# Kernel tuning notes

Measured on AMD Instinct MI355X. Metric: run time of the kernel, lower is better.

Reference implementation:

```python
import jax, jax.numpy as jnp
import numpy as np

NUM_HEADS = 16
BLOCK = 64  # block_size = min(64, N)

def setup_inputs() -> dict:
    key = jax.random.key(0)
    k0, k1, k2 = jax.random.split(key, 3)
    B, N, C = 2, 2048, 1024
    x = jax.random.normal(k0, (B, N, C), dtype=jnp.float32)
    w_qkv = jax.random.normal(k1, (3 * C, C), dtype=jnp.float32) * 0.02  # torch Linear weight [out,in]
    w_proj = jax.random.normal(k2, (C, C), dtype=jnp.float32) * 0.02
    b_proj = jnp.zeros((C,), dtype=jnp.float32)
    return {"x": x, "w_qkv": w_qkv, "w_proj": w_proj, "b_proj": b_proj}

def reference(x, w_qkv, w_proj, b_proj):
    B, N, C = x.shape
    H = NUM_HEADS
    hd = C // H
    bs = min(BLOCK, N)
    scale = hd ** -0.5
    # qkv projection: [B,N,3C] -> [3,B,H,N,hd]
    qkv = (x @ w_qkv.T).reshape(B, N, 3, H, hd).transpose(2, 0, 3, 1, 4)
    q, k, v = qkv[0], qkv[1], qkv[2]
    # block-causal mask: query block i attends to all key blocks <= i
    blk = jnp.arange(N) // bs
    mask = blk[:, None] >= blk[None, :]  # [N,N]
    scores = jnp.einsum('bhqd,bhkd->bhqk', q, k) * scale
    scores = jnp.where(mask, scores, -jnp.inf)
    weights = jax.nn.softmax(scores, axis=-1)
    out = jnp.einsum('bhqk,bhkd->bhqd', weights, v)
    out = out.transpose(0, 2, 1, 3).reshape(B, N, C)
    return out @ w_proj.T + b_proj
```

## Files before the change

kernel.cpp:

```cpp
#include <hip/hip_runtime.h>

typedef __attribute__((ext_vector_type(8))) short bf16x8;
typedef __attribute__((ext_vector_type(4))) float f32x4;
typedef __attribute__((ext_vector_type(2))) unsigned int u32x2;
typedef __attribute__((ext_vector_type(8))) unsigned short ushort8v;

__device__ __forceinline__ unsigned short f2bf(float f) {
  unsigned int u = __float_as_uint(f);
  u += 0x7fffu + ((u >> 16) & 1u);
  return (unsigned short)(u >> 16);
}

__device__ __forceinline__ void gload_lds16(const unsigned short* g, unsigned short* l) {
  __builtin_amdgcn_global_load_lds(
      (const __attribute__((address_space(1))) unsigned int*)g,
      (__attribute__((address_space(3))) unsigned int*)l,
      16, 0, 0);
}

__global__ void cvt_all(const float* __restrict__ x, const float* __restrict__ wq,
                        const float* __restrict__ wp, unsigned short* __restrict__ dst) {
  const int n1 = 4096 * 1024 / 8, n2 = 3072 * 1024 / 8, n3 = 1024 * 1024 / 8;
  int stride = gridDim.x * blockDim.x;
  for (int i = blockIdx.x * blockDim.x + threadIdx.x; i < n1 + n2 + n3; i += stride) {
    const float* s; int j;
    if (i < n1)           { s = x;  j = i; }
    else if (i < n1 + n2) { s = wq; j = i - n1; }
    else                  { s = wp; j = i - n1 - n2; }
    float4 a = ((const float4*)s)[j * 2];
    float4 b = ((const float4*)s)[j * 2 + 1];
    ushort8v o;
    o[0] = f2bf(a.x); o[1] = f2bf(a.y); o[2] = f2bf(a.z); o[3] = f2bf(a.w);
    o[4] = f2bf(b.x); o[5] = f2bf(b.y); o[6] = f2bf(b.z); o[7] = f2bf(b.w);
    ((ushort8v*)dst)[i] = o;
  }
}

__device__ __forceinline__ void gemm128_bt(const unsigned short* __restrict__ A,
                                           const unsigned short* __restrict__ Bt,
                                           unsigned short* As, unsigned short* Bs,
                                           int tm, int tn, f32x4 acc[4][4]) {
  const int K = 1024;
  int tid = threadIdx.x;
  int w = tid >> 6, l = tid & 63;
  int wr = w >> 1, wc = w & 1;
  int g = l >> 4, c = l & 15;

  int srow = w * 32 + (l >> 2);
  int skoff = (((l & 3) ^ ((srow >> 1) & 3)) * 8);
  const unsigned short* gA = A + (size_t)(tm * 128 + srow) * K + skoff;
  const unsigned short* gB = Bt + (size_t)(tn * 128 + srow) * K + skoff;
  unsigned short* lA = As + (w * 32) * 32;
  unsigned short* lB = Bs + (w * 32) * 32;

  int rx = (c >> 1) & 3;
  int arow = wr * 64 + c;
  int brow = wc * 64 + c;

  for (int k0 = 0; k0 < K; k0 += 32) {
    gload_lds16(gA, lA);
    gload_lds16(gA + 16 * K, lA + 16 * 32);
    gload_lds16(gB, lB);
    gload_lds16(gB + 16 * K, lB + 16 * 32);
    gA += 32; gB += 32;
    __syncthreads();
    bf16x8 af[4], bfr[4];
#pragma unroll
    for (int mi = 0; mi < 4; ++mi)
      af[mi] = *(const bf16x8*)((const char*)As + (arow + mi * 16) * 64 + ((g ^ rx) << 4));
#pragma unroll
    for (int ni = 0; ni < 4; ++ni)
      bfr[ni] = *(const bf16x8*)((const char*)Bs + (brow + ni * 16) * 64 + ((g ^ rx) << 4));
#pragma unroll
    for (int mi = 0; mi < 4; ++mi)
#pragma unroll
      for (int ni = 0; ni < 4; ++ni)
        acc[mi][ni] = __builtin_amdgcn_mfma_f32_16x16x32_bf16(af[mi], bfr[ni], acc[mi][ni], 0, 0, 0);
    __syncthreads();
  }
}

__global__ __launch_bounds__(256) void qkv_gemm(const unsigned short* __restrict__ xb,
                                                const unsigned short* __restrict__ wb,
                                                unsigned short* __restrict__ Qp,
                                                unsigned short* __restrict__ Kp,
                                                unsigned short* __restrict__ Vt) {
  __shared__ unsigned short As[128 * 32];
  __shared__ unsigned short Bs[128 * 32];
  f32x4 acc[4][4];
#pragma unroll
  for (int i = 0; i < 4; ++i)
#pragma unroll
    for (int j = 0; j < 4; ++j) acc[i][j] = f32x4{0.f, 0.f, 0.f, 0.f};
  int id = (blockIdx.x & 7) * 96 + (blockIdx.x >> 3);
  int tm = id / 24, tn = id % 24;
  gemm128_bt(xb, wb, As, Bs, tm, tn, acc);

  int tid = threadIdx.x;
  int w = tid >> 6, l = tid & 63;
  int wr = w >> 1, wc = w & 1;
  int g = l >> 4, c = l & 15;
  const float QSCALE = 0.125f * 1.44269504088896f;
#pragma unroll
  for (int mi = 0; mi < 4; ++mi)
#pragma unroll
    for (int ni = 0; ni < 4; ++ni)
#pragma unroll
      for (int r = 0; r < 4; ++r) {
        int row = tm * 128 + wr * 64 + mi * 16 + g * 4 + r;
        int col = tn * 128 + wc * 64 + ni * 16 + c;
        int b = row >> 11, seq = row & 2047;
        int t = col >> 10;
        int h = (col >> 6) & 15, d = col & 63;
        size_t bh = (size_t)b * 16 + h;
        float v = acc[mi][ni][r];
        if (t == 0)      Qp[(bh * 2048 + seq) * 64 + d] = f2bf(v * QSCALE);
        else if (t == 1) Kp[(bh * 2048 + seq) * 64 + d] = f2bf(v);
        else             Vt[(bh * 64 + d) * 2048 + seq] = f2bf(v);
      }
}

__global__ __launch_bounds__(256, 3) void attn_fa(const unsigned short* __restrict__ Qp,
                                                  const unsigned short* __restrict__ Kp,
                                                  const unsigned short* __restrict__ Vt,
                                                  unsigned short* __restrict__ attn) {
  __shared__ unsigned short Ks[2][4096];
  __shared__ unsigned short Vs[2][4096];
  int tid = threadIdx.x;
  int w = tid >> 6, l = tid & 63;
  int g = l >> 4, c = l & 15;

  int idx = blockIdx.x;
  int pos = idx >> 3;
  int qb = 31 - (pos >> 2);
  int bh = (idx & 7) + 8 * (pos & 3);

  const unsigned short* Qbh = Qp + (size_t)bh * 2048 * 64;
  const unsigned short* Kbh = Kp + (size_t)bh * 2048 * 64;
  const unsigned short* Vbh = Vt + (size_t)bh * 64 * 2048;

  int rowA, colA, rowB, colB;
  { int L = tid * 16;         int P = L ^ (((L >> 7) & 7) << 4); rowA = P >> 7; colA = (P & 127) >> 1; }
  { int L = (tid + 256) * 16; int P = L ^ (((L >> 7) & 7) << 4); rowB = P >> 7; colB = (P & 127) >> 1; }
  const unsigned short* gKA = Kbh + rowA * 64 + colA;
  const unsigned short* gKB = Kbh + rowB * 64 + colB;
  const unsigned short* gVA = Vbh + (size_t)rowA * 2048 + colA;
  const unsigned short* gVB = Vbh + (size_t)rowB * 2048 + colB;

#define STAGE(buf, kb)                                              \
  do {                                                              \
    gload_lds16(gKA + (kb) * 4096, &Ks[(buf)][w * 512]);            \
    gload_lds16(gKB + (kb) * 4096, &Ks[(buf)][w * 512 + 2048]);     \
    gload_lds16(gVA + (kb) * 64,  &Vs[(buf)][w * 512]);             \
    gload_lds16(gVB + (kb) * 64,  &Vs[(buf)][w * 512 + 2048]);      \
  } while (0)

  bf16x8 qf[2];
  {
    size_t qrow = (size_t)qb * 64 + w * 16 + c;
    qf[0] = *(const bf16x8*)(Qbh + qrow * 64 + 8 * g);
    qf[1] = *(const bf16x8*)(Qbh + qrow * 64 + 32 + 8 * g);
  }

  float lp4[4] = {0.f, 0.f, 0.f, 0.f};
  f32x4 o[4];
#pragma unroll
  for (int df = 0; df < 4; ++df) o[df] = f32x4{0.f, 0.f, 0.f, 0.f};

  int xorv = c & 7;

  int cur = 0;
  STAGE(0, 0);
  __syncthreads();
  for (int kb = 0; kb <= qb; ++kb) {
    if (kb < qb) STAGE(1 - cur, kb + 1);

    const char* Kb = (const char*)&Ks[cur][0];
    const char* Vb = (const char*)&Vs[cur][0];
    bf16x8 kf[8];
#pragma unroll
    for (int nf = 0; nf < 4; ++nf) {
      int r = nf * 16 + c;
#pragma unroll
      for (int ks = 0; ks < 2; ++ks)
        kf[nf * 2 + ks] = *(const bf16x8*)(Kb + r * 128 + (((ks * 4 + g) ^ xorv) * 16));
    }
    f32x4 s4[4];
#pragma unroll
    for (int nf = 0; nf < 4; ++nf) {
      s4[nf] = f32x4{0.f, 0.f, 0.f, 0.f};
      s4[nf] = __builtin_amdgcn_mfma_f32_16x16x32_bf16(kf[nf * 2 + 0], qf[0], s4[nf], 0, 0, 0);
      s4[nf] = __builtin_amdgcn_mfma_f32_16x16x32_bf16(kf[nf * 2 + 1], qf[1], s4[nf], 0, 0, 0);
    }
    u32x2 pa[4];
#pragma unroll
    for (int nf = 0; nf < 4; ++nf) {
      float p0 = __builtin_amdgcn_exp2f(s4[nf][0]);
      float p1 = __builtin_amdgcn_exp2f(s4[nf][1]);
      float p2 = __builtin_amdgcn_exp2f(s4[nf][2]);
      float p3 = __builtin_amdgcn_exp2f(s4[nf][3]);
      lp4[nf] += (p0 + p1) + (p2 + p3);
      unsigned int w0, w1;
      asm("v_cvt_pk_bf16_f32 %0, %1, %2" : "=v"(w0) : "v"(p0), "v"(p1));
      asm("v_cvt_pk_bf16_f32 %0, %1, %2" : "=v"(w1) : "v"(p2), "v"(p3));
      pa[nf][0] = w0; pa[nf][1] = w1;
    }
#pragma unroll
    for (int df = 0; df < 4; ++df) {
      int vrow = df * 16 + c;
#pragma unroll
      for (int ks = 0; ks < 4; ++ks) {
        u32x2 vbf = *(const u32x2*)(Vb + vrow * 128 + (((2 * ks + (g >> 1)) ^ xorv) * 16) + 8 * (g & 1));
        asm("v_mfma_f32_16x16x16_bf16 %0, %1, %2, %0"
            : "+v"(o[df]) : "v"(pa[ks]), "v"(vbf));
      }
    }
    __syncthreads();
    cur ^= 1;
  }
#undef STAGE

  float lp = (lp4[0] + lp4[1]) + (lp4[2] + lp4[3]);
  lp += __shfl_xor(lp, 16);
  lp += __shfl_xor(lp, 32);
  float inv[4];
#pragma unroll
  for (int r = 0; r < 4; ++r) inv[r] = __builtin_amdgcn_rcpf(__shfl(lp, g * 4 + r));

  int b = bh >> 4, h = bh & 15;
#pragma unroll
  for (int df = 0; df < 4; ++df)
#pragma unroll
    for (int r = 0; r < 4; ++r) {
      int row = qb * 64 + w * 16 + g * 4 + r;
      int colc = h * 64 + df * 16 + c;
      attn[((size_t)b * 2048 + row) * 1024 + colc] = f2bf(o[df][r] * inv[r]);
    }
}

__global__ __launch_bounds__(256) void proj_gemm(const unsigned short* __restrict__ attn,
                                                 const unsigned short* __restrict__ wpb,
                                                 const float* __restrict__ bias,
                                                 float* __restrict__ out) {
  __shared__ unsigned short As[128 * 32];
  __shared__ unsigned short Bs[128 * 32];
  f32x4 acc[4][4];
#pragma unroll
  for (int i = 0; i < 4; ++i)
#pragma unroll
    for (int j = 0; j < 4; ++j) acc[i][j] = f32x4{0.f, 0.f, 0.f, 0.f};
  int id = (blockIdx.x & 7) * 32 + (blockIdx.x >> 3);
  int tm = id / 8, tn = id % 8;
  gemm128_bt(attn, wpb, As, Bs, tm, tn, acc);

  int tid = threadIdx.x;
  int w = tid >> 6, l = tid & 63;
  int wr = w >> 1, wc = w & 1;
  int g = l >> 4, c = l & 15;
#pragma unroll
  for (int mi = 0; mi < 4; ++mi)
#pragma unroll
    for (int ni = 0; ni < 4; ++ni)
#pragma unroll
      for (int r = 0; r < 4; ++r) {
        int row = tm * 128 + wr * 64 + mi * 16 + g * 4 + r;
        int col = tn * 128 + wc * 64 + ni * 16 + c;
        out[(size_t)row * 1024 + col] = acc[mi][ni][r] + bias[col];
      }
}

extern "C" void kernel_launch(void* const* d_in, const int* in_sizes, int n_in,
                              void* d_out, int out_size, void* d_ws, size_t ws_size,
                              hipStream_t stream) {
  (void)in_sizes; (void)n_in; (void)out_size; (void)ws_size;
  const float* x      = (const float*)d_in[0];
  const float* w_qkv  = (const float*)d_in[1];
  const float* w_proj = (const float*)d_in[2];
  const float* b_proj = (const float*)d_in[3];
  float* out = (float*)d_out;

  unsigned short* xb    = (unsigned short*)d_ws;
  unsigned short* wqkvb = xb + 4096 * 1024;
  unsigned short* wpb   = wqkvb + 3072 * 1024;
  unsigned short* Qp    = wpb + 1024 * 1024;
  unsigned short* Kp    = Qp + 32 * 2048 * 64;
  unsigned short* Vt    = Kp + 32 * 2048 * 64;
  unsigned short* attn  = Vt + 32 * 64 * 2048;

  cvt_all<<<1024, 256, 0, stream>>>(x, w_qkv, w_proj, xb);
  qkv_gemm<<<768, 256, 0, stream>>>(xb, wqkvb, Qp, Kp, Vt);
  attn_fa<<<1024, 256, 0, stream>>>(Qp, Kp, Vt, attn);
  proj_gemm<<<256, 256, 0, stream>>>(attn, wpb, b_proj, out);
}
```

Before: 109.7 us.

## Split attention key block across waves and reduce partial outputs through LDS

The attention kernel changes its work split. Each wave previously owned 16 query rows against all 64 keys of a tile. Now each wave owns 16 keys and processes all 64 query rows, so every wave loads one K fragment and four V fragments per tile instead of eight K and sixteen V reads. The cost is four times as many output accumulators in registers, plus a final cross-wave reduction of partial outputs and row sums through LDS, serialized by a loop of syncthreads. Register pressure and lower occupancy may offset the cut in LDS traffic.

```diff
diff --git a/kernel.cpp b/kernel.cpp
--- a/kernel.cpp
+++ b/kernel.cpp
@@ -155,19 +155,23 @@
     gload_lds16(gVB + (kb) * 64,  &Vs[(buf)][w * 512 + 2048]);      \
   } while (0)
 
-  bf16x8 qf[2];
-  {
-    size_t qrow = (size_t)qb * 64 + w * 16 + c;
-    qf[0] = *(const bf16x8*)(Qbh + qrow * 64 + 8 * g);
-    qf[1] = *(const bf16x8*)(Qbh + qrow * 64 + 32 + 8 * g);
+  bf16x8 qf[4][2];
+#pragma unroll
+  for (int qg = 0; qg < 4; ++qg) {
+    size_t qrow = (size_t)qb * 64 + qg * 16 + c;
+    qf[qg][0] = *(const bf16x8*)(Qbh + qrow * 64 + 8 * g);
+    qf[qg][1] = *(const bf16x8*)(Qbh + qrow * 64 + 32 + 8 * g);
   }
 
   float lp4[4] = {0.f, 0.f, 0.f, 0.f};
-  f32x4 o[4];
-#pragma unroll
-  for (int df = 0; df < 4; ++df) o[df] = f32x4{0.f, 0.f, 0.f, 0.f};
+  f32x4 o[4][4];
+#pragma unroll
+  for (int qg = 0; qg < 4; ++qg)
+#pragma unroll
+    for (int df = 0; df < 4; ++df) o[qg][df] = f32x4{0.f, 0.f, 0.f, 0.f};
 
   int xorv = c & 7;
+  int krow = w * 16 + c;
 
   int cur = 0;
   STAGE(0, 0);
@@ -177,64 +181,86 @@
 
     const char* Kb = (const char*)&Ks[cur][0];
     const char* Vb = (const char*)&Vs[cur][0];
-    bf16x8 kf[8];
-#pragma unroll
-    for (int nf = 0; nf < 4; ++nf) {
-      int r = nf * 16 + c;
-#pragma unroll
-      for (int ks = 0; ks < 2; ++ks)
-        kf[nf * 2 + ks] = *(const bf16x8*)(Kb + r * 128 + (((ks * 4 + g) ^ xorv) * 16));
-    }
-    f32x4 s4[4];
-#pragma unroll
-    for (int nf = 0; nf < 4; ++nf) {
-      s4[nf] = f32x4{0.f, 0.f, 0.f, 0.f};
-      s4[nf] = __builtin_amdgcn_mfma_f32_16x16x32_bf16(kf[nf * 2 + 0], qf[0], s4[nf], 0, 0, 0);
-      s4[nf] = __builtin_amdgcn_mfma_f32_16x16x32_bf16(kf[nf * 2 + 1], qf[1], s4[nf], 0, 0, 0);
-    }
+    bf16x8 kf0 = *(const bf16x8*)(Kb + krow * 128 + (((0 * 4 + g) ^ xorv) * 16));
+    bf16x8 kf1 = *(const bf16x8*)(Kb + krow * 128 + (((1 * 4 + g) ^ xorv) * 16));
+    u32x2 vf[4];
+#pragma unroll
+    for (int df = 0; df < 4; ++df)
+      vf[df] = *(const u32x2*)(Vb + (df * 16 + c) * 128 + (((2 * w + (g >> 1)) ^ xorv) * 16) + 8 * (g & 1));
     u32x2 pa[4];
 #pragma unroll
-    for (int nf = 0; nf < 4; ++nf) {
-      float p0 = __builtin_amdgcn_exp2f(s4[nf][0]);
-      float p1 = __builtin_amdgcn_exp2f(s4[nf][1]);
-      float p2 = __builtin_amdgcn_exp2f(s4[nf][2]);
-      float p3 = __builtin_amdgcn_exp2f(s4[nf][3]);
-      lp4[nf] += (p0 + p1) + (p2 + p3);
+    for (int qg = 0; qg < 4; ++qg) {
+      f32x4 s4 = f32x4{0.f, 0.f, 0.f, 0.f};
+      s4 = __builtin_amdgcn_mfma_f32_16x16x32_bf16(kf0, qf[qg][0], s4, 0, 0, 0);
+      s4 = __builtin_amdgcn_mfma_f32_16x16x32_bf16(kf1, qf[qg][1], s4, 0, 0, 0);
+      float p0 = __builtin_amdgcn_exp2f(s4[0]);
+      float p1 = __builtin_amdgcn_exp2f(s4[1]);
+      float p2 = __builtin_amdgcn_exp2f(s4[2]);
+      float p3 = __builtin_amdgcn_exp2f(s4[3]);
+      lp4[qg] += (p0 + p1) + (p2 + p3);
       unsigned int w0, w1;
       asm("v_cvt_pk_bf16_f32 %0, %1, %2" : "=v"(w0) : "v"(p0), "v"(p1));
       asm("v_cvt_pk_bf16_f32 %0, %1, %2" : "=v"(w1) : "v"(p2), "v"(p3));
-      pa[nf][0] = w0; pa[nf][1] = w1;
+      pa[qg][0] = w0; pa[qg][1] = w1;
     }
 #pragma unroll
-    for (int df = 0; df < 4; ++df) {
-      int vrow = df * 16 + c;
-#pragma unroll
-      for (int ks = 0; ks < 4; ++ks) {
-        u32x2 vbf = *(const u32x2*)(Vb + vrow * 128 + (((2 * ks + (g >> 1)) ^ xorv) * 16) + 8 * (g & 1));
+    for (int qg = 0; qg < 4; ++qg)
+#pragma unroll
+      for (int df = 0; df < 4; ++df)
         asm("v_mfma_f32_16x16x16_bf16 %0, %1, %2, %0"
-            : "+v"(o[df]) : "v"(pa[ks]), "v"(vbf));
-      }
+            : "+v"(o[qg][df]) : "v"(pa[qg]), "v"(vf[df]));
+    __syncthreads();
+    cur ^= 1;
+  }
+#undef STAGE
+
+  float* Ored  = (float*)&Ks[0][0];
+  float* lpred = (float*)&Vs[0][0];
+
+  float lpw[4];
+#pragma unroll
+  for (int qg = 0; qg < 4; ++qg) {
+    float v = lp4[qg];
+    v += __shfl_xor(v, 16);
+    v += __shfl_xor(v, 32);
+    lpw[qg] = v;
+  }
+  if (g == 0) {
+#pragma unroll
+    for (int qg = 0; qg < 4; ++qg) lpred[w * 64 + qg * 16 + c] = lpw[qg];
+  }
+  for (int ww = 0; ww < 4; ++ww) {
+    if (w == ww) {
+#pragma unroll
+      for (int qg = 0; qg < 4; ++qg)
+#pragma unroll
+        for (int df = 0; df < 4; ++df)
+#pragma unroll
+          for (int r = 0; r < 4; ++r) {
+            int q = qg * 16 + 4 * g + r, d = df * 16 + c;
+            if (ww == 0) Ored[q * 64 + d] = o[qg][df][r];
+            else         Ored[q * 64 + d] += o[qg][df][r];
+          }
     }
     __syncthreads();
-    cur ^= 1;
-  }
-#undef STAGE
-
-  float lp = (lp4[0] + lp4[1]) + (lp4[2] + lp4[3]);
-  lp += __shfl_xor(lp, 16);
-  lp += __shfl_xor(lp, 32);
+  }
+
   float inv[4];
 #pragma unroll
-  for (int r = 0; r < 4; ++r) inv[r] = __builtin_amdgcn_rcpf(__shfl(lp, g * 4 + r));
-
+  for (int r = 0; r < 4; ++r) {
+    int q = w * 16 + g * 4 + r;
+    float s = (lpred[q] + lpred[64 + q]) + (lpred[128 + q] + lpred[192 + q]);
+    inv[r] = __builtin_amdgcn_rcpf(s);
+  }
   int b = bh >> 4, h = bh & 15;
 #pragma unroll
   for (int df = 0; df < 4; ++df)
 #pragma unroll
     for (int r = 0; r < 4; ++r) {
-      int row = qb * 64 + w * 16 + g * 4 + r;
+      int q = w * 16 + g * 4 + r;
+      int row = qb * 64 + q;
       int colc = h * 64 + df * 16 + c;
-      attn[((size_t)b * 2048 + row) * 1024 + colc] = f2bf(o[df][r] * inv[r]);
+      attn[((size_t)b * 2048 + row) * 1024 + colc] = f2bf(Ored[q * 64 + df * 16 + c] * inv[r]);
     }
 }
 
```

New measurement: 108.9 us. About the same (-0.8%).
